# Kernel optimization log

Hardware: AMD Instinct MI355X
Metric: run time of the kernel (lower is better)

## Reference

```python
import jax, jax.numpy as jnp
import numpy as np

T, H, I, E, TOP_K = 4096, 2048, 1024, 16, 2
I_SHARED = 1024  # moe_intermediate_size * n_shared_experts


def _silu_and_mul(gu):
    g, u = jnp.split(gu, 2, axis=-1)
    return jax.nn.silu(g) * u


def setup_inputs() -> dict:
    key = jax.random.key(0)
    ks = jax.random.split(key, 8)
    s = 0.02
    return {
        "hidden_states": jax.random.normal(ks[0], (T, H), jnp.float32),
        "gate_w": jax.random.normal(ks[1], (E, H), jnp.float32) * s,          # router
        "w1": jax.random.normal(ks[2], (E, 2 * I, H), jnp.float32) * s,       # expert gate_up
        "b1": jax.random.normal(ks[3], (E, 2 * I), jnp.float32) * s,
        "w2": jax.random.normal(ks[4], (E, H, I), jnp.float32) * s,           # expert down
        "sg_w": jax.random.normal(ks[5], (2 * I_SHARED, H), jnp.float32) * s, # shared gate_up
        "sg_b": jax.random.normal(ks[6], (2 * I_SHARED,), jnp.float32) * s,
        "sd_w": jax.random.normal(ks[7], (H, I_SHARED), jnp.float32) * s,     # shared down
    }


def reference(hidden_states, gate_w, w1, b1, w2, sg_w, sg_b, sd_w):
    x = hidden_states  # [T, H]

    # shared expert MLP (gate_up has bias, down does not)
    shared = _silu_and_mul(x @ sg_w.T + sg_b) @ sd_w.T  # [T, H]

    # router: softmax -> top-k -> renormalize (norm_topk_prob=True)
    probs = jax.nn.softmax(x @ gate_w.T, axis=-1)       # [T, E]
    wts, idx = jax.lax.top_k(probs, TOP_K)              # [T, k]
    wts = wts / jnp.sum(wts, axis=-1, keepdims=True)

    # per-expert combine coefficient: coef[e, t] = sum_k wts[t,k] * (idx[t,k]==e)
    coef = jnp.sum(jax.nn.one_hot(idx, E, dtype=x.dtype) * wts[..., None], axis=1).T  # [E, T]

    def body(acc, params):
        w1e, b1e, w2e, ce = params
        a = _silu_and_mul(x @ w1e.T + b1e)   # [T, I]
        return acc + ce[:, None] * (a @ w2e.T), None

    out, _ = jax.lax.scan(body, jnp.zeros_like(x), (w1, b1, w2, coef))
    return out + shared
```

## Files before the change

### kernel.cpp

```cpp
#include <hip/hip_runtime.h>
#include <hip/hip_bf16.h>
#include <stdint.h>

#define T_TOK 4096
#define H_DIM 2048
#define I_DIM 1024
#define NEXP  16
#define NROWS 16384

typedef short bf16x8 __attribute__((ext_vector_type(8)));
typedef float f32x4  __attribute__((ext_vector_type(4)));
typedef unsigned short u16;

__device__ __forceinline__ u16 f2b(float f) {
  union { __hip_bfloat16 h; u16 u; } cv;
  cv.h = __float2bfloat16(f);
  return cv.u;
}

__device__ __forceinline__ void gload16(const void* g, void* l) {
  __builtin_amdgcn_global_load_lds((const __attribute__((address_space(1))) void*)g,
                                   (__attribute__((address_space(3))) void*)l, 16, 0, 0);
}

__device__ __forceinline__ bf16x8 cvt_frag(const float* p) {
  f32x4 v0 = *(const f32x4*)p;
  f32x4 v1 = *(const f32x4*)(p + 4);
  bf16x8 o;
  o[0] = (short)f2b(v0[0]); o[1] = (short)f2b(v0[1]);
  o[2] = (short)f2b(v0[2]); o[3] = (short)f2b(v0[3]);
  o[4] = (short)f2b(v1[0]); o[5] = (short)f2b(v1[1]);
  o[6] = (short)f2b(v1[2]); o[7] = (short)f2b(v1[3]);
  return o;
}

__global__ __launch_bounds__(256) void router_kernel(const float* __restrict__ x,
                                                     const float* __restrict__ gw,
                                                     int* __restrict__ sel,
                                                     float* __restrict__ selw,
                                                     int* __restrict__ counts,
                                                     u16* __restrict__ x_bf) {
  int t = blockIdx.x;
  int tid = threadIdx.x;
  const float* xr = x + (size_t)t * H_DIM;
  double p[NEXP];
#pragma unroll
  for (int e = 0; e < NEXP; ++e) p[e] = 0.0;
  bf16x8 xs;
#pragma unroll
  for (int j = 0; j < 8; ++j) {
    int h = tid * 8 + j;
    float xf = xr[h];
    xs[j] = (short)f2b(xf);
    double xv = (double)xf;
#pragma unroll
    for (int e = 0; e < NEXP; ++e) p[e] += xv * (double)gw[e * H_DIM + h];
  }
  *(bf16x8*)(x_bf + (size_t)t * H_DIM + tid * 8) = xs;
#pragma unroll
  for (int e = 0; e < NEXP; ++e) {
#pragma unroll
    for (int off = 32; off > 0; off >>= 1) p[e] += __shfl_down(p[e], off);
  }
  __shared__ double sm[4][NEXP];
  int w = tid >> 6;
  if ((tid & 63) == 0) {
#pragma unroll
    for (int e = 0; e < NEXP; ++e) sm[w][e] = p[e];
  }
  __syncthreads();
  if (tid == 0) {
    double l0 = -1e300, l1 = -1e300;
    int e0 = 0, e1 = 0;
    for (int e = 0; e < NEXP; ++e) {
      double v = sm[0][e] + sm[1][e] + sm[2][e] + sm[3][e];
      if (v > l0) { l1 = l0; e1 = e0; l0 = v; e0 = e; }
      else if (v > l1) { l1 = v; e1 = e; }
    }
    double w0 = 1.0 / (1.0 + exp(l1 - l0));
    sel[t * 2 + 0] = e0;
    sel[t * 2 + 1] = e1;
    selw[t * 2 + 0] = (float)w0;
    selw[t * 2 + 1] = (float)(1.0 - w0);
    atomicAdd(&counts[e0], 1);
    atomicAdd(&counts[e1], 1);
  }
}

__global__ void prefix_kernel(const int* __restrict__ counts, int* __restrict__ rowbase) {
  if (threadIdx.x == 0 && blockIdx.x == 0) {
    int acc = 0;
    for (int e = 0; e < NEXP; ++e) {
      rowbase[e] = acc;
      acc += (counts[e] + 127) & ~127;
    }
    rowbase[NEXP] = acc;
  }
}

__global__ __launch_bounds__(256) void scatter_kernel(const int* __restrict__ sel,
                                                      const float* __restrict__ selw,
                                                      const int* __restrict__ rowbase,
                                                      int* __restrict__ cursor,
                                                      int* __restrict__ tok_of_row,
                                                      float* __restrict__ coef_of_row) {
  int idx = blockIdx.x * 256 + threadIdx.x;
  if (idx < T_TOK * 2) {
    int t = idx >> 1;
    int e = sel[idx];
    int slot = atomicAdd(&cursor[e], 1);
    int row = rowbase[e] + slot;
    tok_of_row[row] = t;
    coef_of_row[row] = selw[idx];
  } else if (idx < T_TOK * 3) {
    int t = idx - T_TOK * 2;
    int sb = rowbase[NEXP];
    tok_of_row[sb + t] = t;
    coef_of_row[sb + t] = 1.0f;
  }
}


__global__ __launch_bounds__(256, 3) void gemm1_kernel(
    const u16* __restrict__ x_bf, const float* __restrict__ w1,
    const float* __restrict__ sg_w,
    const float* __restrict__ b1, const float* __restrict__ sg_b,
    const int* __restrict__ tok_of_row, const int* __restrict__ counts,
    const int* __restrict__ rowbase, u16* __restrict__ abuf) {
  int nt = blockIdx.x, rt = blockIdx.y, e = blockIdx.z;
  int n_e = (e < NEXP) ? counts[e] : T_TOK;
  if (rt * 128 >= n_e) return;
  int rbase = rowbase[e];
  int n_valid = n_e - rt * 128;
  if (n_valid > 128) n_valid = 128;

  __shared__ short As[128 * 64];
  __shared__ float Bsf[128 * 64];
  __shared__ int Ts[128];

  int tid = threadIdx.x;
  if (tid < 128)
    Ts[tid] = (rt * 128 + tid < n_e) ? tok_of_row[rbase + rt * 128 + tid] : 0;
  __syncthreads();

  int wavebase = tid & 0xC0;
  const u16* srcA[4];
  short* dstA[4];
#pragma unroll
  for (int p = 0; p < 4; ++p) {
    int c = p * 256 + tid;
    int r = c >> 3;
    int koff = ((c & 7) * 8) ^ ((r & 7) << 3);
    int tok = Ts[r];
    srcA[p] = x_bf + (size_t)tok * H_DIM + koff;
    dstA[p] = &As[(p * 256 + wavebase) * 8];
  }
  const float* Wexp = (e < NEXP) ? (w1 + (size_t)e * (2 * I_DIM) * H_DIM) : sg_w;
  const float* srcB[8];
  float* dstB[8];
#pragma unroll
  for (int p = 0; p < 8; ++p) {
    int c = p * 256 + tid;
    int r = c >> 4;
    int eoff = ((c & 15) ^ (2 * (r & 7))) * 4;
    int gr = (r < 64) ? (nt * 64 + r) : (I_DIM + nt * 64 + (r - 64));
    srcB[p] = Wexp + (size_t)gr * H_DIM + eoff;
    dstB[p] = &Bsf[(p * 256 + wavebase) * 4];
  }

  f32x4 acc[4][4];
#pragma unroll
  for (int m = 0; m < 4; ++m)
#pragma unroll
    for (int n = 0; n < 4; ++n) acc[m][n] = (f32x4){0.f, 0.f, 0.f, 0.f};

  int lane = tid & 63, w = tid >> 6, wr = w >> 1, wc = w & 1;
  int laneq = lane & 15, hi = lane >> 4;

  for (int kt = 0; kt < H_DIM / 64; ++kt) {
    if (kt) __syncthreads();
#pragma unroll
    for (int p = 0; p < 4; ++p) gload16(srcA[p] + kt * 64, dstA[p]);
#pragma unroll
    for (int p = 0; p < 8; ++p) gload16(srcB[p] + kt * 64, dstB[p]);
    __syncthreads();
#pragma unroll
    for (int ks = 0; ks < 2; ++ks) {
      bf16x8 a[4], b[4];
#pragma unroll
      for (int f = 0; f < 4; ++f) {
        int rowA = wr * 64 + f * 16 + laneq;
        a[f] = *(const bf16x8*)(As + rowA * 64 + ((ks * 32 + hi * 8) ^ ((rowA & 7) << 3)));
        int rowB = ((f < 2) ? (wc * 32 + f * 16) : (64 + wc * 32 + (f - 2) * 16)) + laneq;
        int cc = (ks * 8 + hi * 2) ^ (2 * (rowB & 7));
        b[f] = cvt_frag(Bsf + rowB * 64 + cc * 4);
      }
#pragma unroll
      for (int f = 0; f < 4; ++f)
#pragma unroll
        for (int fn = 0; fn < 4; ++fn)
          acc[f][fn] = __builtin_amdgcn_mfma_f32_16x16x32_bf16(a[f], b[fn], acc[f][fn], 0, 0, 0);
    }
  }

  const float* bias = (e < NEXP) ? (b1 + (size_t)e * (2 * I_DIM)) : sg_b;
#pragma unroll
  for (int nf = 0; nf < 2; ++nf) {
    int j = nt * 64 + wc * 32 + nf * 16 + laneq;
    float bg = bias[j];
    float bu = bias[I_DIM + j];
#pragma unroll
    for (int mf = 0; mf < 4; ++mf) {
#pragma unroll
      for (int reg = 0; reg < 4; ++reg) {
        int r = wr * 64 + mf * 16 + hi * 4 + reg;
        if (r < n_valid) {
          float g = acc[mf][nf][reg] + bg;
          float u = acc[mf][nf + 2][reg] + bu;
          float s = g / (1.0f + __expf(-g));
          abuf[(size_t)(rbase + rt * 128 + r) * I_DIM + j] = f2b(s * u);
        }
      }
    }
  }
}

template <int ATOMIC>
__global__ __launch_bounds__(256, 3) void gemm2_kernel(
    const u16* __restrict__ abuf, const float* __restrict__ w2,
    const float* __restrict__ sd_w,
    const int* __restrict__ tok_of_row, const float* __restrict__ coef_of_row,
    const int* __restrict__ counts, const int* __restrict__ rowbase,
    float* __restrict__ out, int e_force) {
  int nt = blockIdx.x, rt = blockIdx.y;
  int e = (e_force >= 0) ? e_force : (int)blockIdx.z;
  int n_e = (e < NEXP) ? counts[e] : T_TOK;
  if (rt * 128 >= n_e) return;
  int rbase = rowbase[e];
  int n_valid = n_e - rt * 128;
  if (n_valid > 128) n_valid = 128;

  __shared__ short As[128 * 64];
  __shared__ float Bsf[128 * 64];
  __shared__ int Ts[128];
  __shared__ float Cs[128];

  int tid = threadIdx.x;
  if (tid < 128) {
    bool valid = rt * 128 + tid < n_e;
    int row = rbase + rt * 128 + tid;
    Ts[tid] = valid ? tok_of_row[row] : 0;
    Cs[tid] = valid ? coef_of_row[row] : 0.0f;
  }
  __syncthreads();

  int wavebase = tid & 0xC0;
  const u16* srcA[4];
  short* dstA[4];
#pragma unroll
  for (int p = 0; p < 4; ++p) {
    int c = p * 256 + tid;
    int r = c >> 3;
    int koff = ((c & 7) * 8) ^ ((r & 7) << 3);
    srcA[p] = abuf + (size_t)(rbase + rt * 128 + r) * I_DIM + koff;
    dstA[p] = &As[(p * 256 + wavebase) * 8];
  }
  const float* Wexp = (e < NEXP) ? (w2 + (size_t)e * H_DIM * I_DIM) : sd_w;
  const float* srcB[8];
  float* dstB[8];
#pragma unroll
  for (int p = 0; p < 8; ++p) {
    int c = p * 256 + tid;
    int r = c >> 4;
    int eoff = ((c & 15) ^ (2 * (r & 7))) * 4;
    srcB[p] = Wexp + (size_t)(nt * 128 + r) * I_DIM + eoff;
    dstB[p] = &Bsf[(p * 256 + wavebase) * 4];
  }

  f32x4 acc[4][4];
#pragma unroll
  for (int m = 0; m < 4; ++m)
#pragma unroll
    for (int n = 0; n < 4; ++n) acc[m][n] = (f32x4){0.f, 0.f, 0.f, 0.f};

  int lane = tid & 63, w = tid >> 6, wr = w >> 1, wc = w & 1;
  int laneq = lane & 15, hi = lane >> 4;

  for (int kt = 0; kt < I_DIM / 64; ++kt) {
    if (kt) __syncthreads();
#pragma unroll
    for (int p = 0; p < 4; ++p) gload16(srcA[p] + kt * 64, dstA[p]);
#pragma unroll
    for (int p = 0; p < 8; ++p) gload16(srcB[p] + kt * 64, dstB[p]);
    __syncthreads();
#pragma unroll
    for (int ks = 0; ks < 2; ++ks) {
      bf16x8 a[4], b[4];
#pragma unroll
      for (int f = 0; f < 4; ++f) {
        int rowA = wr * 64 + f * 16 + laneq;
        int rowB = wc * 64 + f * 16 + laneq;
        a[f] = *(const bf16x8*)(As + rowA * 64 + ((ks * 32 + hi * 8) ^ ((rowA & 7) << 3)));
        int cc = (ks * 8 + hi * 2) ^ (2 * (rowB & 7));
        b[f] = cvt_frag(Bsf + rowB * 64 + cc * 4);
      }
#pragma unroll
      for (int f = 0; f < 4; ++f)
#pragma unroll
        for (int fn = 0; fn < 4; ++fn)
          acc[f][fn] = __builtin_amdgcn_mfma_f32_16x16x32_bf16(a[f], b[fn], acc[f][fn], 0, 0, 0);
    }
  }

#pragma unroll
  for (int mf = 0; mf < 4; ++mf) {
#pragma unroll
    for (int nf = 0; nf < 4; ++nf) {
      int col = nt * 128 + wc * 64 + nf * 16 + laneq;
#pragma unroll
      for (int reg = 0; reg < 4; ++reg) {
        int r = wr * 64 + mf * 16 + hi * 4 + reg;
        if (r < n_valid) {
          int tok = Ts[r];
          float val = acc[mf][nf][reg] * Cs[r];
          float* p = out + (size_t)tok * H_DIM + col;
          if (ATOMIC) atomicAdd(p, val);
          else *p = val;
        }
      }
    }
  }
}

extern "C" void kernel_launch(void* const* d_in, const int* in_sizes, int n_in,
                              void* d_out, int out_size, void* d_ws, size_t ws_size,
                              hipStream_t stream) {
  const float* x    = (const float*)d_in[0];
  const float* gate_w = (const float*)d_in[1];
  const float* w1   = (const float*)d_in[2];
  const float* b1   = (const float*)d_in[3];
  const float* w2   = (const float*)d_in[4];
  const float* sg_w = (const float*)d_in[5];
  const float* sg_b = (const float*)d_in[6];
  const float* sd_w = (const float*)d_in[7];
  float* out = (float*)d_out;

  uint8_t* ws = (uint8_t*)d_ws;
  size_t off = 0;
  auto alloc = [&](size_t bytes) -> void* {
    void* p = ws + off;
    off += (bytes + 255) & ~(size_t)255;
    return p;
  };
  u16*  x_bf  = (u16*)alloc((size_t)T_TOK * H_DIM * 2);
  u16*  abuf  = (u16*)alloc((size_t)NROWS * I_DIM * 2);
  int*  tok_of_row  = (int*)alloc((size_t)NROWS * 4);
  float* coef_of_row = (float*)alloc((size_t)NROWS * 4);
  int*  sel   = (int*)alloc((size_t)T_TOK * 2 * 4);
  float* selw = (float*)alloc((size_t)T_TOK * 2 * 4);
  int*  counts  = (int*)alloc(256);
  int*  cursor  = (int*)alloc(256);
  int*  rowbase = (int*)alloc(256);
  (void)ws_size; (void)in_sizes; (void)n_in; (void)out_size;

  hipMemsetAsync(counts, 0, 512, stream);

  router_kernel<<<dim3(T_TOK), dim3(256), 0, stream>>>(x, gate_w, sel, selw, counts, x_bf);
  prefix_kernel<<<dim3(1), dim3(64), 0, stream>>>(counts, rowbase);
  scatter_kernel<<<dim3(48), dim3(256), 0, stream>>>(sel, selw, rowbase, cursor, tok_of_row, coef_of_row);

  gemm1_kernel<<<dim3(16, 32, 17), dim3(256), 0, stream>>>(
      x_bf, w1, sg_w, b1, sg_b, tok_of_row, counts, rowbase, abuf);

  gemm2_kernel<0><<<dim3(16, 32, 1), dim3(256), 0, stream>>>(
      abuf, w2, sd_w, tok_of_row, coef_of_row, counts, rowbase, out, NEXP);
  gemm2_kernel<1><<<dim3(16, 32, 16), dim3(256), 0, stream>>>(
      abuf, w2, sd_w, tok_of_row, coef_of_row, counts, rowbase, out, -1);
}
```

Measured before the change: 474.1 us.

## Widen LDS swizzle for fp32 B tiles and merge gemm2 launches via zeroed atomics

```diff
diff --git a/kernel.cpp b/kernel.cpp
--- a/kernel.cpp
+++ b/kernel.cpp
@@ -23,9 +23,9 @@
                                    (__attribute__((address_space(3))) void*)l, 16, 0, 0);
 }
 
-__device__ __forceinline__ bf16x8 cvt_frag(const float* p) {
-  f32x4 v0 = *(const f32x4*)p;
-  f32x4 v1 = *(const f32x4*)(p + 4);
+__device__ __forceinline__ bf16x8 cvt_frag2(const float* pLo, const float* pHi) {
+  f32x4 v0 = *(const f32x4*)pLo;
+  f32x4 v1 = *(const f32x4*)pHi;
   bf16x8 o;
   o[0] = (short)f2b(v0[0]); o[1] = (short)f2b(v0[1]);
   o[2] = (short)f2b(v0[2]); o[3] = (short)f2b(v0[3]);
@@ -162,7 +162,7 @@
   for (int p = 0; p < 8; ++p) {
     int c = p * 256 + tid;
     int r = c >> 4;
-    int eoff = ((c & 15) ^ (2 * (r & 7))) * 4;
+    int eoff = ((c & 15) ^ (r & 15)) * 4;
     int gr = (r < 64) ? (nt * 64 + r) : (I_DIM + nt * 64 + (r - 64));
     srcB[p] = Wexp + (size_t)gr * H_DIM + eoff;
     dstB[p] = &Bsf[(p * 256 + wavebase) * 4];
@@ -192,8 +192,9 @@
         int rowA = wr * 64 + f * 16 + laneq;
         a[f] = *(const bf16x8*)(As + rowA * 64 + ((ks * 32 + hi * 8) ^ ((rowA & 7) << 3)));
         int rowB = ((f < 2) ? (wc * 32 + f * 16) : (64 + wc * 32 + (f - 2) * 16)) + laneq;
-        int cc = (ks * 8 + hi * 2) ^ (2 * (rowB & 7));
-        b[f] = cvt_frag(Bsf + rowB * 64 + cc * 4);
+        int s0 = (ks * 8 + hi * 2) ^ (rowB & 15);
+        const float* pB = Bsf + rowB * 64;
+        b[f] = cvt_frag2(pB + s0 * 4, pB + (s0 ^ 1) * 4);
       }
 #pragma unroll
       for (int f = 0; f < 4; ++f)
@@ -225,15 +226,13 @@
   }
 }
 
-template <int ATOMIC>
 __global__ __launch_bounds__(256, 3) void gemm2_kernel(
     const u16* __restrict__ abuf, const float* __restrict__ w2,
     const float* __restrict__ sd_w,
     const int* __restrict__ tok_of_row, const float* __restrict__ coef_of_row,
     const int* __restrict__ counts, const int* __restrict__ rowbase,
-    float* __restrict__ out, int e_force) {
-  int nt = blockIdx.x, rt = blockIdx.y;
-  int e = (e_force >= 0) ? e_force : (int)blockIdx.z;
+    float* __restrict__ out) {
+  int nt = blockIdx.x, rt = blockIdx.y, e = blockIdx.z;
   int n_e = (e < NEXP) ? counts[e] : T_TOK;
   if (rt * 128 >= n_e) return;
   int rbase = rowbase[e];
@@ -272,7 +271,7 @@
   for (int p = 0; p < 8; ++p) {
     int c = p * 256 + tid;
     int r = c >> 4;
-    int eoff = ((c & 15) ^ (2 * (r & 7))) * 4;
+    int eoff = ((c & 15) ^ (r & 15)) * 4;
     srcB[p] = Wexp + (size_t)(nt * 128 + r) * I_DIM + eoff;
     dstB[p] = &Bsf[(p * 256 + wavebase) * 4];
   }
@@ -301,8 +300,9 @@
         int rowA = wr * 64 + f * 16 + laneq;
         int rowB = wc * 64 + f * 16 + laneq;
         a[f] = *(const bf16x8*)(As + rowA * 64 + ((ks * 32 + hi * 8) ^ ((rowA & 7) << 3)));
-        int cc = (ks * 8 + hi * 2) ^ (2 * (rowB & 7));
-        b[f] = cvt_frag(Bsf + rowB * 64 + cc * 4);
+        int s0 = (ks * 8 + hi * 2) ^ (rowB & 15);
+        const float* pB = Bsf + rowB * 64;
+        b[f] = cvt_frag2(pB + s0 * 4, pB + (s0 ^ 1) * 4);
       }
 #pragma unroll
       for (int f = 0; f < 4; ++f)
@@ -322,10 +322,7 @@
         int r = wr * 64 + mf * 16 + hi * 4 + reg;
         if (r < n_valid) {
           int tok = Ts[r];
-          float val = acc[mf][nf][reg] * Cs[r];
-          float* p = out + (size_t)tok * H_DIM + col;
-          if (ATOMIC) atomicAdd(p, val);
-          else *p = val;
+          atomicAdd(out + (size_t)tok * H_DIM + col, acc[mf][nf][reg] * Cs[r]);
         }
       }
     }
@@ -364,6 +361,7 @@
   (void)ws_size; (void)in_sizes; (void)n_in; (void)out_size;
 
   hipMemsetAsync(counts, 0, 512, stream);
+  hipMemsetAsync(out, 0, (size_t)T_TOK * H_DIM * 4, stream);
 
   router_kernel<<<dim3(T_TOK), dim3(256), 0, stream>>>(x, gate_w, sel, selw, counts, x_bf);
   prefix_kernel<<<dim3(1), dim3(64), 0, stream>>>(counts, rowbase);
@@ -372,8 +370,6 @@
   gemm1_kernel<<<dim3(16, 32, 17), dim3(256), 0, stream>>>(
       x_bf, w1, sg_w, b1, sg_b, tok_of_row, counts, rowbase, abuf);
 
-  gemm2_kernel<0><<<dim3(16, 32, 1), dim3(256), 0, stream>>>(
-      abuf, w2, sd_w, tok_of_row, coef_of_row, counts, rowbase, out, NEXP);
-  gemm2_kernel<1><<<dim3(16, 32, 16), dim3(256), 0, stream>>>(
-      abuf, w2, sd_w, tok_of_row, coef_of_row, counts, rowbase, out, -1);
-}
+  gemm2_kernel<<<dim3(16, 32, 17), dim3(256), 0, stream>>>(
+      abuf, w2, sd_w, tok_of_row, coef_of_row, counts, rowbase, out);
+}
```

After: 469.4 us. About the same (-1.0%).
